# Kernel tuning notes

Measured on AMD Instinct MI355X. Metric: run time of the kernel, lower is better.

## Reference

```python
import jax, jax.numpy as jnp
import numpy as np

MARGIN = 1.0  # cur_margin for LBA_inverted_loss=True
COS_SCALE = 128.0


def smoothed_metric_loss(X, margin=MARGIN):
    # X: [B, E]. Lifted structured loss with inverted cosine similarity.
    B = X.shape[0]
    P = B // 2
    D = (X @ X.T) / COS_SCALE            # [B, B]
    E = jnp.exp(margin + D)              # [B, B]
    # For pair p (rows i=2p, j=2p+1): sum E over rows {i,j}, all columns except {i,j}.
    Eb = E.reshape(P, 2, P, 2)           # [P, 2, P, 2]
    row_sums = Eb.sum(axis=(1, 2, 3))    # [P] full sum over both rows of pair p
    idx = jnp.arange(P)
    diag_block = Eb[idx, :, idx, :].sum(axis=(1, 2))  # [P] the excluded 2x2 block
    S = row_sums - diag_block            # [P] masked sums
    Dij = D.reshape(P, 2, P, 2)[idx, 0, idx, 1]       # [P] D[i, j]
    J = jnp.log(S) - Dij
    return 0.5 * jnp.mean(J * J)


def reference(text_embeddings, shape_embeddings):
    B = text_embeddings.shape[0]
    # shape_embeddings repeated twice per model: row k -> shape[k // 2]
    shape_rep = jnp.repeat(shape_embeddings, 2, axis=0)      # [B, E]
    metric_tt = smoothed_metric_loss(text_embeddings)
    # mask rows: even rows keep text, odd rows take repeated shape embedding
    even = (jnp.arange(B) % 2 == 0)[:, None]
    mixed = jnp.where(even, text_embeddings, shape_rep)      # [B, E]
    metric_st = smoothed_metric_loss(mixed)
    return metric_tt + metric_st


def setup_inputs() -> dict:
    key = jax.random.key(0)
    k1, k2 = jax.random.split(key)
    B, E = 8192, 128
    text_embeddings = jax.random.normal(k1, (B, E), dtype=jnp.float32)
    shape_embeddings = jax.random.normal(k2, (B // 2, E), dtype=jnp.float32)
    return {"text_embeddings": text_embeddings, "shape_embeddings": shape_embeddings}
```

## Files before the change

kernel.cpp:

```cpp
#include <hip/hip_runtime.h>
#include <hip/hip_bf16.h>


#define B_ROWS 8192
#define E_COLS 128
#define P_PAIRS 4096
#define NSTRIP 128
#define NH 8

using f32x4 = __attribute__((ext_vector_type(4))) float;
using i32x8 = __attribute__((ext_vector_type(8))) int;

#define BF_SCALE 0.106164482742544f
#define EULER    2.718281828459045f
#define SCALE1   0x7f

__device__ __forceinline__ unsigned pk4_fp8(float a, float b, float c, float d) {
    unsigned v = 0;
    v = __builtin_amdgcn_cvt_pk_fp8_f32(a * BF_SCALE, b * BF_SCALE, v, false);
    v = __builtin_amdgcn_cvt_pk_fp8_f32(c * BF_SCALE, d * BF_SCALE, v, true);
    return v;
}

__global__ void convert_kernel(const float* __restrict__ text,
                               const float* __restrict__ shape,
                               unsigned* __restrict__ Xt,
                               unsigned* __restrict__ Xm,
                               float* __restrict__ R,
                               float* __restrict__ out) {
    int idx = blockIdx.x * blockDim.x + threadIdx.x;
    if (idx < 4096) {
        float4 z; z.x = z.y = z.z = z.w = 0.f;
        ((float4*)R)[idx] = z;
    }
    if (idx == 0) *out = 0.f;
    int e = idx * 4;
    if (e >= B_ROWS * E_COLS) return;
    float4 t = *(const float4*)(text + e);
    unsigned tp = pk4_fp8(t.x, t.y, t.z, t.w);
    Xt[idx] = tp;
    int row = e >> 7;
    if (row & 1) {
        int col = e & 127;
        float4 s = *(const float4*)(shape + (row >> 1) * E_COLS + col);
        Xm[idx] = pk4_fp8(s.x, s.y, s.z, s.w);
    } else {
        Xm[idx] = tp;
    }
}

__device__ __forceinline__ int lds_off(int row, int k0) {
    return (row << 7) + (k0 ^ ((row & 7) << 4));
}

__device__ __forceinline__ i32x8 load_frag32(const char* base, int row, int k32) {
    union { i32x8 v; int4 h[2]; } u;
    u.h[0] = *(const int4*)(base + lds_off(row, k32));
    u.h[1] = *(const int4*)(base + lds_off(row, k32 + 16));
    return u.v;
}

__device__ __forceinline__ void stage8k(const char* gsrc, char* ldst, int tid) {
#pragma unroll
    for (int it = 0; it < 2; ++it) {
        int L   = it * 4096 + tid * 16;
        int row = L >> 7;
        int cb  = L & 127;
        int src = (row << 7) + (cb ^ ((row & 7) << 4));
        __builtin_amdgcn_global_load_lds(
            (const __attribute__((address_space(1))) void*)(gsrc + src),
            (__attribute__((address_space(3))) void*)(ldst + L), 16, 0, 0);
    }
}

__launch_bounds__(256, 6)
__global__ void gemm_rowsum_kernel(const unsigned char* __restrict__ Xt,
                                   const unsigned char* __restrict__ Xm,
                                   float* __restrict__ R) {
    const int bm = blockIdx.x, h = blockIdx.y, l = blockIdx.z;
    const char* gX = (const char*)(l ? Xm : Xt);

    __shared__ __align__(16) char buf0[64 * 128];
    __shared__ __align__(16) char buf1[64 * 128];
    const int tid = threadIdx.x;

    const int t0 = (h == 0) ? NH : h;
    const int N  = (h == 0) ? (bm < 64 ? 8 : 7) : 8;

    stage8k(gX + bm * 8192, buf0, tid);
    stage8k(gX + ((bm + t0) & 127) * 8192, buf1, tid);
    asm volatile("s_waitcnt vmcnt(2)" ::: "memory");
    __builtin_amdgcn_s_barrier();

    const int lane = tid & 63;
    const int w  = tid >> 6;
    const int wr = w >> 1, wc = w & 1;
    const int rA0 = wr * 32 + (lane & 15);
    const int rB0 = wc * 32 + (lane & 15);
    const int k32 = (lane >> 4) * 32;

    i32x8 afr[2];
#pragma unroll
    for (int m = 0; m < 2; ++m)
        afr[m] = load_frag32(buf0, rA0 + m * 16, k32);

    float s_r[2][4] = {{0.f}};

    if (h == 0) {
        i32x8 bfr[2];
#pragma unroll
        for (int n = 0; n < 2; ++n)
            bfr[n] = load_frag32(buf0, rB0 + n * 16, k32);
        f32x4 acc[2][2] = {};
#pragma unroll
        for (int m = 0; m < 2; ++m)
#pragma unroll
            for (int n = 0; n < 2; ++n)
                acc[m][n] = __builtin_amdgcn_mfma_scale_f32_16x16x128_f8f6f4(
                    afr[m], bfr[n], acc[m][n], 0, 0, 0, SCALE1, 0, SCALE1);
#pragma unroll
        for (int m = 0; m < 2; ++m)
#pragma unroll
            for (int n = 0; n < 2; ++n)
#pragma unroll
                for (int j = 0; j < 4; ++j)
                    s_r[m][j] += __builtin_amdgcn_exp2f(acc[m][n][j]);
    }

    asm volatile("s_waitcnt lgkmcnt(0)" ::: "memory");
    __builtin_amdgcn_s_barrier();

    int cur = 1;
    for (int idx = 0; idx < N; ++idx) {
        const bool hasnext = (idx + 1 < N);
        if (hasnext)
            stage8k(gX + ((bm + t0 + NH * (idx + 1)) & 127) * 8192,
                    cur ? buf0 : buf1, tid);

        if (hasnext) { asm volatile("s_waitcnt vmcnt(2)" ::: "memory"); }
        else         { asm volatile("s_waitcnt vmcnt(0)" ::: "memory"); }
        __builtin_amdgcn_s_barrier();

        const char* lsrc = cur ? buf1 : buf0;
        i32x8 bfr[2];
#pragma unroll
        for (int n = 0; n < 2; ++n)
            bfr[n] = load_frag32(lsrc, rB0 + n * 16, k32);
        f32x4 acc[2][2] = {};
#pragma unroll
        for (int m = 0; m < 2; ++m)
#pragma unroll
            for (int n = 0; n < 2; ++n)
                acc[m][n] = __builtin_amdgcn_mfma_scale_f32_16x16x128_f8f6f4(
                    afr[m], bfr[n], acc[m][n], 0, 0, 0, SCALE1, 0, SCALE1);

        asm volatile("s_waitcnt lgkmcnt(0)" ::: "memory");
        __builtin_amdgcn_s_barrier();

        const int bn = (bm + t0 + NH * idx) & 127;
        float s_c[2] = {0.f, 0.f};
#pragma unroll
        for (int m = 0; m < 2; ++m)
#pragma unroll
            for (int n = 0; n < 2; ++n)
#pragma unroll
                for (int j = 0; j < 4; ++j) {
                    float e2 = __builtin_amdgcn_exp2f(acc[m][n][j]);
                    s_r[m][j] += e2;
                    s_c[n] += e2;
                }
#pragma unroll
        for (int n = 0; n < 2; ++n) {
            float v = s_c[n];
            v += __shfl_xor(v, 16, 64);
            v += __shfl_xor(v, 32, 64);
            if (lane < 16) {
                int gcol = bn * 64 + wc * 32 + n * 16 + lane;
                atomicAdd(&R[l * B_ROWS + gcol], EULER * v);
            }
        }
        cur ^= 1;
    }

#pragma unroll
    for (int m = 0; m < 2; ++m)
#pragma unroll
        for (int j = 0; j < 4; ++j) {
            float v = s_r[m][j];
            v += __shfl_xor(v, 1, 64);
            v += __shfl_xor(v, 2, 64);
            v += __shfl_xor(v, 4, 64);
            v += __shfl_xor(v, 8, 64);
            if ((lane & 15) == 0) {
                int grow = bm * 64 + wr * 32 + m * 16 + (lane >> 4) * 4 + j;
                atomicAdd(&R[l * B_ROWS + grow], EULER * v);
            }
        }
}

__global__ void finalize_kernel(const float* __restrict__ text,
                                const float* __restrict__ shape,
                                const float* __restrict__ R,
                                float* __restrict__ out) {
    const int tid = threadIdx.x;
    const int lane = tid & 63;
    const int w = tid >> 6;
    const int waveGlobal = blockIdx.x * 4 + w;
    const float inv128 = 0.0078125f;
    float accum = 0.f;

    for (int task = waveGlobal; task < 2 * P_PAIRS; task += 1024) {
        int l = task >> 12;
        int p = task & (P_PAIRS - 1);
        const float* a = text + (2 * p) * E_COLS;
        const float* b = l ? (shape + p * E_COLS) : (text + (2 * p + 1) * E_COLS);
        float2 av = *(const float2*)(a + lane * 2);
        float2 bv = *(const float2*)(b + lane * 2);
        float dii = av.x * av.x + av.y * av.y;
        float djj = bv.x * bv.x + bv.y * bv.y;
        float dij = av.x * bv.x + av.y * bv.y;
#pragma unroll
        for (int sh = 1; sh < 64; sh <<= 1) {
            dii += __shfl_xor(dii, sh, 64);
            djj += __shfl_xor(djj, sh, 64);
            dij += __shfl_xor(dij, sh, 64);
        }
        if (lane == 0) {
            float Dii = dii * inv128, Djj = djj * inv128, Dij = dij * inv128;
            float S = R[l * B_ROWS + 2 * p] + R[l * B_ROWS + 2 * p + 1]
                    - (__expf(1.f + Dii) + 2.f * __expf(1.f + Dij) + __expf(1.f + Djj));
            float J = __logf(S) - Dij;
            accum += 0.5f * J * J * (1.0f / (float)P_PAIRS);
        }
    }

    __shared__ float red[4];
    if (lane == 0) red[w] = accum;
    __syncthreads();
    if (tid == 0) {
        atomicAdd(out, red[0] + red[1] + red[2] + red[3]);
    }
}

extern "C" void kernel_launch(void* const* d_in, const int* in_sizes, int n_in,
                              void* d_out, int out_size, void* d_ws, size_t ws_size,
                              hipStream_t stream) {
    const float* text  = (const float*)d_in[0];
    const float* shape = (const float*)d_in[1];
    float* out = (float*)d_out;
    char* ws = (char*)d_ws;

    unsigned char* Xt = (unsigned char*)ws;
    unsigned char* Xm = (unsigned char*)(ws + 1u * 1024u * 1024u);
    float* R = (float*)(ws + 2u * 1024u * 1024u);

    convert_kernel<<<(B_ROWS * E_COLS / 4 + 255) / 256, 256, 0, stream>>>(
        text, shape, (unsigned*)Xt, (unsigned*)Xm, R, out);

    dim3 grid(NSTRIP, NH, 2);
    gemm_rowsum_kernel<<<grid, 256, 0, stream>>>(Xt, Xm, R);

    finalize_kernel<<<256, 256, 0, stream>>>(text, shape, R, out);
}
```

Before: 42.43 us.

## Triple-buffer B tiles, load A fragments from global, one barrier per step

The GEMM-rowsum kernel moves from double to triple LDS buffering with a prefetch distance of two tiles, which leaves one barrier per iteration instead of two. The A fragments and the diagonal-block B fragments are now read straight from global memory instead of being staged through LDS. MFMA issue is wrapped in s_setprio, and the finalize kernel is launched with twice as many blocks and a matching loop stride. LDS use rises to 24KB per block, which may limit occupancy, and the vmcnt bookkeeping is more fragile.

```diff
diff --git a/kernel.cpp b/kernel.cpp
--- a/kernel.cpp
+++ b/kernel.cpp
@@ -60,6 +60,13 @@
     return u.v;
 }
 
+__device__ __forceinline__ i32x8 load_frag32_g(const char* rowbase, int k32) {
+    union { i32x8 v; int4 h[2]; } u;
+    u.h[0] = *(const int4*)(rowbase + k32);
+    u.h[1] = *(const int4*)(rowbase + k32 + 16);
+    return u.v;
+}
+
 __device__ __forceinline__ void stage8k(const char* gsrc, char* ldst, int tid) {
 #pragma unroll
     for (int it = 0; it < 2; ++it) {
@@ -80,17 +87,14 @@
     const int bm = blockIdx.x, h = blockIdx.y, l = blockIdx.z;
     const char* gX = (const char*)(l ? Xm : Xt);
 
-    __shared__ __align__(16) char buf0[64 * 128];
-    __shared__ __align__(16) char buf1[64 * 128];
+    __shared__ __align__(16) char bufs[3][64 * 128];
     const int tid = threadIdx.x;
 
     const int t0 = (h == 0) ? NH : h;
     const int N  = (h == 0) ? (bm < 64 ? 8 : 7) : 8;
 
-    stage8k(gX + bm * 8192, buf0, tid);
-    stage8k(gX + ((bm + t0) & 127) * 8192, buf1, tid);
-    asm volatile("s_waitcnt vmcnt(2)" ::: "memory");
-    __builtin_amdgcn_s_barrier();
+    stage8k(gX + (size_t)((bm + t0) & 127) * 8192, bufs[0], tid);
+    stage8k(gX + (size_t)((bm + t0 + NH) & 127) * 8192, bufs[1], tid);
 
     const int lane = tid & 63;
     const int w  = tid >> 6;
@@ -99,25 +103,25 @@
     const int rB0 = wc * 32 + (lane & 15);
     const int k32 = (lane >> 4) * 32;
 
+    const char* Ag = gX + (size_t)bm * 8192;
     i32x8 afr[2];
-#pragma unroll
-    for (int m = 0; m < 2; ++m)
-        afr[m] = load_frag32(buf0, rA0 + m * 16, k32);
+    afr[0] = load_frag32_g(Ag + (size_t)rA0 * 128, k32);
+    afr[1] = load_frag32_g(Ag + (size_t)(rA0 + 16) * 128, k32);
 
     float s_r[2][4] = {{0.f}};
 
     if (h == 0) {
-        i32x8 bfr[2];
-#pragma unroll
-        for (int n = 0; n < 2; ++n)
-            bfr[n] = load_frag32(buf0, rB0 + n * 16, k32);
+        i32x8 b0 = load_frag32_g(Ag + (size_t)rB0 * 128, k32);
+        i32x8 b1 = load_frag32_g(Ag + (size_t)(rB0 + 16) * 128, k32);
         f32x4 acc[2][2] = {};
-#pragma unroll
-        for (int m = 0; m < 2; ++m)
-#pragma unroll
-            for (int n = 0; n < 2; ++n)
-                acc[m][n] = __builtin_amdgcn_mfma_scale_f32_16x16x128_f8f6f4(
-                    afr[m], bfr[n], acc[m][n], 0, 0, 0, SCALE1, 0, SCALE1);
+        acc[0][0] = __builtin_amdgcn_mfma_scale_f32_16x16x128_f8f6f4(
+            afr[0], b0, acc[0][0], 0, 0, 0, SCALE1, 0, SCALE1);
+        acc[0][1] = __builtin_amdgcn_mfma_scale_f32_16x16x128_f8f6f4(
+            afr[0], b1, acc[0][1], 0, 0, 0, SCALE1, 0, SCALE1);
+        acc[1][0] = __builtin_amdgcn_mfma_scale_f32_16x16x128_f8f6f4(
+            afr[1], b0, acc[1][0], 0, 0, 0, SCALE1, 0, SCALE1);
+        acc[1][1] = __builtin_amdgcn_mfma_scale_f32_16x16x128_f8f6f4(
+            afr[1], b1, acc[1][1], 0, 0, 0, SCALE1, 0, SCALE1);
 #pragma unroll
         for (int m = 0; m < 2; ++m)
 #pragma unroll
@@ -127,35 +131,30 @@
                     s_r[m][j] += __builtin_amdgcn_exp2f(acc[m][n][j]);
     }
 
-    asm volatile("s_waitcnt lgkmcnt(0)" ::: "memory");
+    asm volatile("s_waitcnt vmcnt(0)" ::: "memory");
     __builtin_amdgcn_s_barrier();
 
-    int cur = 1;
     for (int idx = 0; idx < N; ++idx) {
-        const bool hasnext = (idx + 1 < N);
-        if (hasnext)
-            stage8k(gX + ((bm + t0 + NH * (idx + 1)) & 127) * 8192,
-                    cur ? buf0 : buf1, tid);
-
-        if (hasnext) { asm volatile("s_waitcnt vmcnt(2)" ::: "memory"); }
-        else         { asm volatile("s_waitcnt vmcnt(0)" ::: "memory"); }
-        __builtin_amdgcn_s_barrier();
-
-        const char* lsrc = cur ? buf1 : buf0;
+        if (idx + 2 < N)
+            stage8k(gX + (size_t)((bm + t0 + NH * (idx + 2)) & 127) * 8192,
+                    bufs[(idx + 2) % 3], tid);
+
+        const char* lsrc = bufs[idx % 3];
         i32x8 bfr[2];
-#pragma unroll
-        for (int n = 0; n < 2; ++n)
-            bfr[n] = load_frag32(lsrc, rB0 + n * 16, k32);
+        bfr[0] = load_frag32(lsrc, rB0, k32);
+        bfr[1] = load_frag32(lsrc, rB0 + 16, k32);
+
         f32x4 acc[2][2] = {};
-#pragma unroll
-        for (int m = 0; m < 2; ++m)
-#pragma unroll
-            for (int n = 0; n < 2; ++n)
-                acc[m][n] = __builtin_amdgcn_mfma_scale_f32_16x16x128_f8f6f4(
-                    afr[m], bfr[n], acc[m][n], 0, 0, 0, SCALE1, 0, SCALE1);
-
-        asm volatile("s_waitcnt lgkmcnt(0)" ::: "memory");
-        __builtin_amdgcn_s_barrier();
+        __builtin_amdgcn_s_setprio(1);
+        acc[0][0] = __builtin_amdgcn_mfma_scale_f32_16x16x128_f8f6f4(
+            afr[0], bfr[0], acc[0][0], 0, 0, 0, SCALE1, 0, SCALE1);
+        acc[0][1] = __builtin_amdgcn_mfma_scale_f32_16x16x128_f8f6f4(
+            afr[0], bfr[1], acc[0][1], 0, 0, 0, SCALE1, 0, SCALE1);
+        acc[1][0] = __builtin_amdgcn_mfma_scale_f32_16x16x128_f8f6f4(
+            afr[1], bfr[0], acc[1][0], 0, 0, 0, SCALE1, 0, SCALE1);
+        acc[1][1] = __builtin_amdgcn_mfma_scale_f32_16x16x128_f8f6f4(
+            afr[1], bfr[1], acc[1][1], 0, 0, 0, SCALE1, 0, SCALE1);
+        __builtin_amdgcn_s_setprio(0);
 
         const int bn = (bm + t0 + NH * idx) & 127;
         float s_c[2] = {0.f, 0.f};
@@ -179,7 +178,12 @@
                 atomicAdd(&R[l * B_ROWS + gcol], EULER * v);
             }
         }
-        cur ^= 1;
+
+        if (idx + 1 < N) {
+            asm volatile("s_waitcnt lgkmcnt(0)" ::: "memory");
+            asm volatile("s_waitcnt vmcnt(4)" ::: "memory");
+            __builtin_amdgcn_s_barrier();
+        }
     }
 
 #pragma unroll
@@ -209,7 +213,7 @@
     const float inv128 = 0.0078125f;
     float accum = 0.f;
 
-    for (int task = waveGlobal; task < 2 * P_PAIRS; task += 1024) {
+    for (int task = waveGlobal; task < 2 * P_PAIRS; task += 2048) {
         int l = task >> 12;
         int p = task & (P_PAIRS - 1);
         const float* a = text + (2 * p) * E_COLS;
@@ -260,5 +264,5 @@
     dim3 grid(NSTRIP, NH, 2);
     gemm_rowsum_kernel<<<grid, 256, 0, stream>>>(Xt, Xm, R);
 
-    finalize_kernel<<<256, 256, 0, stream>>>(text, shape, R, out);
-}
+    finalize_kernel<<<512, 256, 0, stream>>>(text, shape, R, out);
+}
```

After: 44.54 us. 1.05x slower.

## Fuse convert, GEMM-rowsum and finalize into one cooperative persistent kernel

Applied to the files above, without the earlier changes.

Replaces three kernel launches with one cooperative kernel of 512 blocks. The kernel runs the conversion, the GEMM row-sum over 2048 groups in a grid-stride loop, and the finalize stage, with grid.sync between stages. The aim is to remove launch and inter-kernel gaps. In exchange it adds grid-wide barrier cost, gives the GEMM fewer concurrent blocks (launch bounds go from 6 to 4 blocks per unit), and keeps the old three-kernel path as a fallback if the cooperative launch fails.

```diff
diff --git a/kernel.cpp b/kernel.cpp
--- a/kernel.cpp
+++ b/kernel.cpp
@@ -1,5 +1,8 @@
 #include <hip/hip_runtime.h>
 #include <hip/hip_bf16.h>
+#include <hip/hip_cooperative_groups.h>
+
+namespace cg = cooperative_groups;
 
 
 #define B_ROWS 8192
@@ -7,6 +10,7 @@
 #define P_PAIRS 4096
 #define NSTRIP 128
 #define NH 8
+#define NGROUP 2048
 
 using f32x4 = __attribute__((ext_vector_type(4))) float;
 using i32x8 = __attribute__((ext_vector_type(8))) int;
@@ -22,20 +26,44 @@
     return v;
 }
 
-__global__ void convert_kernel(const float* __restrict__ text,
-                               const float* __restrict__ shape,
-                               unsigned* __restrict__ Xt,
-                               unsigned* __restrict__ Xm,
-                               float* __restrict__ R,
-                               float* __restrict__ out) {
-    int idx = blockIdx.x * blockDim.x + threadIdx.x;
+__device__ __forceinline__ int lds_off(int row, int k0) {
+    return (row << 7) + (k0 ^ ((row & 7) << 4));
+}
+
+__device__ __forceinline__ i32x8 load_frag32(const char* base, int row, int k32) {
+    union { i32x8 v; int4 h[2]; } u;
+    u.h[0] = *(const int4*)(base + lds_off(row, k32));
+    u.h[1] = *(const int4*)(base + lds_off(row, k32 + 16));
+    return u.v;
+}
+
+__device__ __forceinline__ void stage8k(const char* gsrc, char* ldst, int tid) {
+#pragma unroll
+    for (int it = 0; it < 2; ++it) {
+        int L   = it * 4096 + tid * 16;
+        int row = L >> 7;
+        int cb  = L & 127;
+        int src = (row << 7) + (cb ^ ((row & 7) << 4));
+        __builtin_amdgcn_global_load_lds(
+            (const __attribute__((address_space(1))) void*)(gsrc + src),
+            (__attribute__((address_space(3))) void*)(ldst + L), 16, 0, 0);
+    }
+}
+
+
+__device__ __forceinline__ void convert_item(int idx,
+                                             const float* __restrict__ text,
+                                             const float* __restrict__ shape,
+                                             unsigned* __restrict__ Xt,
+                                             unsigned* __restrict__ Xm,
+                                             float* __restrict__ R,
+                                             float* __restrict__ out) {
     if (idx < 4096) {
         float4 z; z.x = z.y = z.z = z.w = 0.f;
         ((float4*)R)[idx] = z;
     }
     if (idx == 0) *out = 0.f;
     int e = idx * 4;
-    if (e >= B_ROWS * E_COLS) return;
     float4 t = *(const float4*)(text + e);
     unsigned tp = pk4_fp8(t.x, t.y, t.z, t.w);
     Xt[idx] = tp;
@@ -49,46 +77,15 @@
     }
 }
 
-__device__ __forceinline__ int lds_off(int row, int k0) {
-    return (row << 7) + (k0 ^ ((row & 7) << 4));
-}
-
-__device__ __forceinline__ i32x8 load_frag32(const char* base, int row, int k32) {
-    union { i32x8 v; int4 h[2]; } u;
-    u.h[0] = *(const int4*)(base + lds_off(row, k32));
-    u.h[1] = *(const int4*)(base + lds_off(row, k32 + 16));
-    return u.v;
-}
-
-__device__ __forceinline__ void stage8k(const char* gsrc, char* ldst, int tid) {
-#pragma unroll
-    for (int it = 0; it < 2; ++it) {
-        int L   = it * 4096 + tid * 16;
-        int row = L >> 7;
-        int cb  = L & 127;
-        int src = (row << 7) + (cb ^ ((row & 7) << 4));
-        __builtin_amdgcn_global_load_lds(
-            (const __attribute__((address_space(1))) void*)(gsrc + src),
-            (__attribute__((address_space(3))) void*)(ldst + L), 16, 0, 0);
-    }
-}
-
-__launch_bounds__(256, 6)
-__global__ void gemm_rowsum_kernel(const unsigned char* __restrict__ Xt,
-                                   const unsigned char* __restrict__ Xm,
-                                   float* __restrict__ R) {
-    const int bm = blockIdx.x, h = blockIdx.y, l = blockIdx.z;
-    const char* gX = (const char*)(l ? Xm : Xt);
-
-    __shared__ __align__(16) char buf0[64 * 128];
-    __shared__ __align__(16) char buf1[64 * 128];
-    const int tid = threadIdx.x;
-
+__device__ __forceinline__ void gemm_group_body(const char* __restrict__ gX,
+                                                float* __restrict__ R,
+                                                int bm, int h, int l, int tid,
+                                                char* buf0, char* buf1) {
     const int t0 = (h == 0) ? NH : h;
     const int N  = (h == 0) ? (bm < 64 ? 8 : 7) : 8;
 
-    stage8k(gX + bm * 8192, buf0, tid);
-    stage8k(gX + ((bm + t0) & 127) * 8192, buf1, tid);
+    stage8k(gX + (size_t)bm * 8192, buf0, tid);
+    stage8k(gX + (size_t)((bm + t0) & 127) * 8192, buf1, tid);
     asm volatile("s_waitcnt vmcnt(2)" ::: "memory");
     __builtin_amdgcn_s_barrier();
 
@@ -134,7 +131,7 @@
     for (int idx = 0; idx < N; ++idx) {
         const bool hasnext = (idx + 1 < N);
         if (hasnext)
-            stage8k(gX + ((bm + t0 + NH * (idx + 1)) & 127) * 8192,
+            stage8k(gX + (size_t)((bm + t0 + NH * (idx + 1)) & 127) * 8192,
                     cur ? buf0 : buf1, tid);
 
         if (hasnext) { asm volatile("s_waitcnt vmcnt(2)" ::: "memory"); }
@@ -198,6 +195,101 @@
         }
 }
 
+__device__ __forceinline__ float finalize_task(int task,
+                                               const float* __restrict__ text,
+                                               const float* __restrict__ shape,
+                                               const float* __restrict__ R,
+                                               int lane) {
+    const float inv128 = 0.0078125f;
+    int l = task >> 12;
+    int p = task & (P_PAIRS - 1);
+    const float* a = text + (2 * p) * E_COLS;
+    const float* b = l ? (shape + p * E_COLS) : (text + (2 * p + 1) * E_COLS);
+    float2 av = *(const float2*)(a + lane * 2);
+    float2 bv = *(const float2*)(b + lane * 2);
+    float dii = av.x * av.x + av.y * av.y;
+    float djj = bv.x * bv.x + bv.y * bv.y;
+    float dij = av.x * bv.x + av.y * bv.y;
+#pragma unroll
+    for (int sh = 1; sh < 64; sh <<= 1) {
+        dii += __shfl_xor(dii, sh, 64);
+        djj += __shfl_xor(djj, sh, 64);
+        dij += __shfl_xor(dij, sh, 64);
+    }
+    float r = 0.f;
+    if (lane == 0) {
+        float Dii = dii * inv128, Djj = djj * inv128, Dij = dij * inv128;
+        float S = R[l * B_ROWS + 2 * p] + R[l * B_ROWS + 2 * p + 1]
+                - (__expf(1.f + Dii) + 2.f * __expf(1.f + Dij) + __expf(1.f + Djj));
+        float J = __logf(S) - Dij;
+        r = 0.5f * J * J * (1.0f / (float)P_PAIRS);
+    }
+    return r;
+}
+
+__launch_bounds__(256, 4)
+__global__ void fused_kernel(const float* __restrict__ text,
+                             const float* __restrict__ shape,
+                             unsigned char* __restrict__ Xt8,
+                             unsigned char* __restrict__ Xm8,
+                             float* __restrict__ R,
+                             float* __restrict__ out) {
+    cg::grid_group grid = cg::this_grid();
+    const int tid = threadIdx.x;
+    const int bid = blockIdx.x;
+    const int nb  = gridDim.x;
+
+    __shared__ __align__(16) char buf0[64 * 128];
+    __shared__ __align__(16) char buf1[64 * 128];
+    __shared__ float red[4];
+
+    for (int idx = bid * 256 + tid; idx < B_ROWS * E_COLS / 4; idx += nb * 256)
+        convert_item(idx, text, shape, (unsigned*)Xt8, (unsigned*)Xm8, R, out);
+    grid.sync();
+
+    for (int g = bid; g < NGROUP; g += nb) {
+        const int bm = g & 127;
+        const int h  = (g >> 7) & 7;
+        const int l  = g >> 10;
+        gemm_group_body((const char*)(l ? Xm8 : Xt8), R, bm, h, l, tid, buf0, buf1);
+        __syncthreads();
+    }
+    grid.sync();
+
+    {
+        const int lane = tid & 63;
+        const int w = tid >> 6;
+        float accum = 0.f;
+        for (int task = bid * 4 + w; task < 2 * P_PAIRS; task += nb * 4)
+            accum += finalize_task(task, text, shape, R, lane);
+        if (lane == 0) red[w] = accum;
+        __syncthreads();
+        if (tid == 0) atomicAdd(out, red[0] + red[1] + red[2] + red[3]);
+    }
+}
+
+__global__ void convert_kernel(const float* __restrict__ text,
+                               const float* __restrict__ shape,
+                               unsigned* __restrict__ Xt,
+                               unsigned* __restrict__ Xm,
+                               float* __restrict__ R,
+                               float* __restrict__ out) {
+    int idx = blockIdx.x * blockDim.x + threadIdx.x;
+    if (idx < B_ROWS * E_COLS / 4)
+        convert_item(idx, text, shape, Xt, Xm, R, out);
+}
+
+__launch_bounds__(256, 4)
+__global__ void gemm_rowsum_kernel(const unsigned char* __restrict__ Xt,
+                                   const unsigned char* __restrict__ Xm,
+                                   float* __restrict__ R) {
+    __shared__ __align__(16) char buf0[64 * 128];
+    __shared__ __align__(16) char buf1[64 * 128];
+    const int bm = blockIdx.x, h = blockIdx.y, l = blockIdx.z;
+    gemm_group_body((const char*)(l ? Xm : Xt), R, bm, h, l, threadIdx.x,
+                    buf0, buf1);
+}
+
 __global__ void finalize_kernel(const float* __restrict__ text,
                                 const float* __restrict__ shape,
                                 const float* __restrict__ R,
@@ -205,41 +297,13 @@
     const int tid = threadIdx.x;
     const int lane = tid & 63;
     const int w = tid >> 6;
-    const int waveGlobal = blockIdx.x * 4 + w;
-    const float inv128 = 0.0078125f;
     float accum = 0.f;
-
-    for (int task = waveGlobal; task < 2 * P_PAIRS; task += 1024) {
-        int l = task >> 12;
-        int p = task & (P_PAIRS - 1);
-        const float* a = text + (2 * p) * E_COLS;
-        const float* b = l ? (shape + p * E_COLS) : (text + (2 * p + 1) * E_COLS);
-        float2 av = *(const float2*)(a + lane * 2);
-        float2 bv = *(const float2*)(b + lane * 2);
-        float dii = av.x * av.x + av.y * av.y;
-        float djj = bv.x * bv.x + bv.y * bv.y;
-        float dij = av.x * bv.x + av.y * bv.y;
-#pragma unroll
-        for (int sh = 1; sh < 64; sh <<= 1) {
-            dii += __shfl_xor(dii, sh, 64);
-            djj += __shfl_xor(djj, sh, 64);
-            dij += __shfl_xor(dij, sh, 64);
-        }
-        if (lane == 0) {
-            float Dii = dii * inv128, Djj = djj * inv128, Dij = dij * inv128;
-            float S = R[l * B_ROWS + 2 * p] + R[l * B_ROWS + 2 * p + 1]
-                    - (__expf(1.f + Dii) + 2.f * __expf(1.f + Dij) + __expf(1.f + Djj));
-            float J = __logf(S) - Dij;
-            accum += 0.5f * J * J * (1.0f / (float)P_PAIRS);
-        }
-    }
-
+    for (int task = blockIdx.x * 4 + w; task < 2 * P_PAIRS; task += 1024)
+        accum += finalize_task(task, text, shape, R, lane);
     __shared__ float red[4];
     if (lane == 0) red[w] = accum;
     __syncthreads();
-    if (tid == 0) {
-        atomicAdd(out, red[0] + red[1] + red[2] + red[3]);
-    }
+    if (tid == 0) atomicAdd(out, red[0] + red[1] + red[2] + red[3]);
 }
 
 extern "C" void kernel_launch(void* const* d_in, const int* in_sizes, int n_in,
@@ -254,11 +318,16 @@
     unsigned char* Xm = (unsigned char*)(ws + 1u * 1024u * 1024u);
     float* R = (float*)(ws + 2u * 1024u * 1024u);
 
-    convert_kernel<<<(B_ROWS * E_COLS / 4 + 255) / 256, 256, 0, stream>>>(
-        text, shape, (unsigned*)Xt, (unsigned*)Xm, R, out);
-
-    dim3 grid(NSTRIP, NH, 2);
-    gemm_rowsum_kernel<<<grid, 256, 0, stream>>>(Xt, Xm, R);
-
-    finalize_kernel<<<256, 256, 0, stream>>>(text, shape, R, out);
-}
+    void* kargs[] = {(void*)&text, (void*)&shape, (void*)&Xt, (void*)&Xm,
+                     (void*)&R, (void*)&out};
+    hipError_t err = hipLaunchCooperativeKernel((const void*)fused_kernel,
+                                                dim3(512), dim3(256),
+                                                kargs, 0, stream);
+    if (err != hipSuccess) {
+        (void)hipGetLastError();
+        convert_kernel<<<(B_ROWS * E_COLS / 4 + 255) / 256, 256, 0, stream>>>(
+            text, shape, (unsigned*)Xt, (unsigned*)Xm, R, out);
+        gemm_rowsum_kernel<<<dim3(NSTRIP, NH, 2), 256, 0, stream>>>(Xt, Xm, R);
+        finalize_kernel<<<256, 256, 0, stream>>>(text, shape, R, out);
+    }
+}
```

Result: slower. 154.5 us (+264.2%).
